# Kernel tuning notes

Hardware: AMD Instinct MI355X
Metric: run time of the kernel (lower is better)

## Reference

```python
import jax, jax.numpy as jnp
import numpy as np

N, K = 50000, 16          # nodes, max degree (subgraph size = K+1)
C_IN, C_HID, C_OUT = 128, 128, 64
T1, T2 = 1.0, 0.5         # evolution_times per layer (used via .item() in torch, i.e. constants)


def setup_inputs() -> dict:
    key = jax.random.key(0)
    kx, kw1, kw2, kd = jax.random.split(key, 4)
    n = jnp.arange(N)
    # distinct, non-self neighbor ids: (n + m_n * j) mod N, m_n*j <= 97*16 < N
    m = 1 + (n % 97)
    j = jnp.arange(1, K + 1)
    neighbors = ((n[:, None] + m[:, None] * j[None, :]) % N).astype(jnp.int32)  # [N,K]
    deg = jax.random.randint(kd, (N,), 4, K + 1)                                # variable degree 4..16
    nbr_mask = jnp.arange(K)[None, :] < deg[:, None]                            # [N,K] bool
    x = jax.random.normal(kx, (N, C_IN), dtype=jnp.float32)
    # xavier-uniform linear weights (bias=False in lin; separate bias param zeros-init)
    lim1 = float(np.sqrt(6.0 / (C_IN + C_HID)))
    lim2 = float(np.sqrt(6.0 / (C_HID + C_OUT)))
    W1 = jax.random.uniform(kw1, (C_HID, C_IN), jnp.float32, -lim1, lim1)
    W2 = jax.random.uniform(kw2, (C_OUT, C_HID), jnp.float32, -lim2, lim2)
    b1 = jnp.zeros((C_HID,), jnp.float32)
    b2 = jnp.zeros((C_OUT,), jnp.float32)
    return {"x": x, "neighbors": neighbors, "nbr_mask": nbr_mask,
            "W1": W1, "b1": b1, "W2": W2, "b2": b2}


def _star_evolution_weights(nbr_mask, t):
    """Per-node unitary-dilation evolution weights Re(G[0,:]) / sqrt(max eig(G G^H)).

    A_i is the star adjacency of the node's incident subgraph (size K+1);
    padded leaves are disconnected so their row-0 weight is exactly 0.
    """
    S = K + 1
    m = nbr_mask.astype(jnp.float32)                       # [N,K]
    A = jnp.zeros((nbr_mask.shape[0], S, S), jnp.float32)
    A = A.at[:, 0, 1:].set(m).at[:, 1:, 0].set(m)          # star adjacency [N,S,S]
    G = jax.vmap(jax.scipy.linalg.expm)((-1j * t) * A.astype(jnp.complex64))  # [N,S,S] c64
    # normalization by sqrt(max eigenvalue of G G^H) (== 1 up to fp error: G unitary)
    GGd = jnp.einsum('nij,nkj->nik', G, jnp.conj(G))
    smax = jnp.sqrt(jnp.max(jnp.linalg.eigvalsh(GGd), axis=-1))              # [N]
    # features are real, only real part of evolved features is kept:
    return jnp.real(G[:, 0, :]) / smax[:, None].astype(jnp.float32)          # [N,S]


def _conv(h, W, b, neighbors, nbr_mask, t):
    ht = h @ W.T                                             # [N,C'] lin (no bias)
    g0 = _star_evolution_weights(nbr_mask, t)                # [N,K+1]
    sub = jnp.concatenate([ht[:, None, :], ht[neighbors]], axis=1)  # [N,K+1,C']
    return jnp.einsum('ns,nsc->nc', g0, sub) + b


def reference(x, neighbors, nbr_mask, W1, b1, W2, b2):
    h = jax.nn.relu(_conv(x, W1, b1, neighbors, nbr_mask, T1))   # dropout: eval mode (no-op)
    o = _conv(h, W2, b2, neighbors, nbr_mask, T2)
    return jax.nn.log_softmax(o, axis=1)
```

## Files before the change

### kernel.cpp

```cpp
#include <hip/hip_runtime.h>
#include <hip/hip_bf16.h>


#define NN    50000
#define CIN   128
#define CHID  128
#define COUT  64
#define KNBR  16
#define TM    64
#define BLOCK 256

typedef unsigned short u16;
typedef unsigned int   u32;
typedef __attribute__((ext_vector_type(8))) short bf16x8;
typedef __attribute__((ext_vector_type(4))) float f32x4;

__device__ __forceinline__ u16 f2bf(float f) {
    __hip_bfloat16 h = __float2bfloat16(f);
    return *reinterpret_cast<u16*>(&h);
}
__device__ __forceinline__ uint4 pack8u(const float* __restrict__ p) {
    float tmp[8];
    *(float4*)(tmp)     = *(const float4*)(p);
    *(float4*)(tmp + 4) = *(const float4*)(p + 4);
    union { u16 h[8]; uint4 v; } r;
    #pragma unroll
    for (int i = 0; i < 8; ++i) r.h[i] = f2bf(tmp[i]);
    return r.v;
}

__device__ __forceinline__ int sw(int row, int g) { return (g ^ (row & 15)) << 3; }

#define WS_CC_OFF 65536

__global__ void wprep(const float* __restrict__ w1g,
                      const float* __restrict__ w2g,
                      uint4* __restrict__ wimg)
{
    int gid = blockIdx.x * BLOCK + threadIdx.x;
    if (gid < 2048) {
        int c = gid >> 4, kg = gid & 15;
        wimg[kg * 128 + c] = pack8u(w1g + c * CIN + kg * 8);
    } else if (gid < 3072) {
        int g2 = gid - 2048;
        int c = g2 >> 4, kg = g2 & 15;
        wimg[2048 + kg * 64 + c] = pack8u(w2g + c * CHID + kg * 8);
    }
}

__global__ void cprep(const int* __restrict__ maskg, float* __restrict__ cc)
{
    int n = blockIdx.x * BLOCK + threadIdx.x;
    if (n < NN) {
        int deg = 0;
        #pragma unroll
        for (int j = 0; j < KNBR; ++j) deg += (maskg[(size_t)n * KNBR + j] != 0);
        float sd = sqrtf((float)deg);
        cc[n]      = cosf(sd);
        cc[NN + n] = cosf(0.5f * sd);
    }
}

__global__ __launch_bounds__(BLOCK, 3)
void gcn_mfma(const float* __restrict__ xg,
              const uint4* __restrict__ wimg,
              const float* __restrict__ cc,
              const float* __restrict__ b1g,
              const float* __restrict__ b2g,
              float* __restrict__ out)
{
    __shared__ __align__(16) char region[17408 + 16384];
    u16*   xt  = (u16*)region;
    float* osc = (float*)region;
    u16*   ht  = (u16*)(region + 17408);

    __shared__ float c1v[TM], c2v[TM], b1l[CHID], b2l[COUT];
    __shared__ float pm[TM * 4], ps[TM * 4], lsev[TM];

    const int t  = threadIdx.x;
    const int w  = t >> 6;
    const int L  = t & 63;
    const int q  = L >> 4;
    const int lm = L & 15;
    const int m0 = blockIdx.x * TM;

    #pragma unroll
    for (int i = 0; i < 4; ++i) {
        int c = t + i * BLOCK;
        int row = c >> 4, g = c & 15;
        int gn = m0 + row;
        uint4 v = make_uint4(0u, 0u, 0u, 0u);
        if (gn < NN) v = pack8u(xg + (size_t)gn * CIN + (g << 3));
        *(uint4*)&xt[row * CIN + sw(row, g)] = v;
    }

    bf16x8 w1f[2][4];
    #pragma unroll
    for (int nt = 0; nt < 2; ++nt) {
        int c = w * 32 + nt * 16 + lm;
        #pragma unroll
        for (int k4 = 0; k4 < 4; ++k4)
            w1f[nt][k4] = *(const bf16x8*)&wimg[(k4 * 4 + q) * 128 + c];
    }

    if (t < CHID) b1l[t] = b1g[t];
    if (t < COUT) b2l[t] = b2g[t];
    if (t < TM) {
        int gn = m0 + t;
        c1v[t] = (gn < NN) ? cc[gn]      : 0.f;
        c2v[t] = (gn < NN) ? cc[NN + gn] : 0.f;
    }
    __syncthreads();

    f32x4 acc[4][2];
    #pragma unroll
    for (int i = 0; i < 4; ++i)
        #pragma unroll
        for (int nt = 0; nt < 2; ++nt)
            acc[i][nt] = (f32x4){0.f, 0.f, 0.f, 0.f};

    #pragma unroll
    for (int k4 = 0; k4 < 4; ++k4) {
        bf16x8 af[4];
        #pragma unroll
        for (int i = 0; i < 4; ++i) {
            int r = i * 16 + lm;
            af[i] = *(const bf16x8*)&xt[r * CIN + sw(r, k4 * 4 + q)];
        }
        #pragma unroll
        for (int i = 0; i < 4; ++i)
            #pragma unroll
            for (int nt = 0; nt < 2; ++nt)
                acc[i][nt] = __builtin_amdgcn_mfma_f32_16x16x32_bf16(
                    af[i], w1f[nt][k4], acc[i][nt], 0, 0, 0);
    }

    #pragma unroll
    for (int i = 0; i < 4; ++i) {
        #pragma unroll
        for (int nt = 0; nt < 2; ++nt) {
            int chan = w * 32 + nt * 16 + lm;
            float bb = b1l[chan];
            #pragma unroll
            for (int r = 0; r < 4; ++r) {
                int node = i * 16 + q * 4 + r;
                float h = fmaxf(fmaf(c1v[node], acc[i][nt][r], bb), 0.f);
                ht[node * CHID + sw(node, chan >> 3) + (chan & 7)] = f2bf(h);
            }
        }
    }

    bf16x8 w2f[4];
    {
        int c = w * 16 + lm;
        #pragma unroll
        for (int k4 = 0; k4 < 4; ++k4)
            w2f[k4] = *(const bf16x8*)&wimg[2048 + (k4 * 4 + q) * 64 + c];
    }
    __syncthreads();

    f32x4 a2[4];
    #pragma unroll
    for (int i = 0; i < 4; ++i) a2[i] = (f32x4){0.f, 0.f, 0.f, 0.f};

    #pragma unroll
    for (int k4 = 0; k4 < 4; ++k4) {
        bf16x8 af[4];
        #pragma unroll
        for (int i = 0; i < 4; ++i) {
            int r = i * 16 + lm;
            af[i] = *(const bf16x8*)&ht[r * CHID + sw(r, k4 * 4 + q)];
        }
        #pragma unroll
        for (int i = 0; i < 4; ++i)
            a2[i] = __builtin_amdgcn_mfma_f32_16x16x32_bf16(
                af[i], w2f[k4], a2[i], 0, 0, 0);
    }

    {
        int chan = w * 16 + lm;
        float bb = b2l[chan];
        #pragma unroll
        for (int i = 0; i < 4; ++i)
            #pragma unroll
            for (int r = 0; r < 4; ++r) {
                int node = i * 16 + q * 4 + r;
                osc[node * 68 + chan] = fmaf(c2v[node], a2[i][r], bb);
            }
    }
    __syncthreads();

    {
        int node = t >> 2, part = t & 3;
        float m = -1e30f;
        #pragma unroll
        for (int qq = 0; qq < 16; ++qq)
            m = fmaxf(m, osc[node * 68 + part * 16 + qq]);
        pm[node * 4 + part] = m;
    }
    __syncthreads();
    {
        int node = t >> 2, part = t & 3;
        float M = fmaxf(fmaxf(pm[node * 4], pm[node * 4 + 1]),
                        fmaxf(pm[node * 4 + 2], pm[node * 4 + 3]));
        float s = 0.f;
        #pragma unroll
        for (int qq = 0; qq < 16; ++qq)
            s += expf(osc[node * 68 + part * 16 + qq] - M);
        ps[node * 4 + part] = s;
        if (part == 0) pm[node * 4] = M;
    }
    __syncthreads();
    {
        int node = t >> 2, part = t & 3;
        if (part == 0)
            lsev[node] = pm[node * 4] +
                logf(ps[node * 4] + ps[node * 4 + 1] + ps[node * 4 + 2] + ps[node * 4 + 3]);
    }
    __syncthreads();

    for (int e4 = t; e4 < TM * COUT / 4; e4 += BLOCK) {
        int n = e4 >> 4;
        if (m0 + n >= NN) break;
        int c0 = (e4 & 15) << 2;
        float l = lsev[n];
        float4 v;
        v.x = osc[n * 68 + c0]     - l;
        v.y = osc[n * 68 + c0 + 1] - l;
        v.z = osc[n * 68 + c0 + 2] - l;
        v.w = osc[n * 68 + c0 + 3] - l;
        *(float4*)(out + (size_t)(m0 + n) * COUT + c0) = v;
    }
}

extern "C" void kernel_launch(void* const* d_in, const int* in_sizes, int n_in,
                              void* d_out, int out_size, void* d_ws, size_t ws_size,
                              hipStream_t stream) {
    const float* x   = (const float*)d_in[0];
    const int* mask  = (const int*)d_in[2];
    const float* w1  = (const float*)d_in[3];
    const float* b1  = (const float*)d_in[4];
    const float* w2  = (const float*)d_in[5];
    const float* b2  = (const float*)d_in[6];
    float* out = (float*)d_out;

    uint4* wimg = (uint4*)d_ws;
    float* cc   = (float*)((char*)d_ws + WS_CC_OFF);

    hipLaunchKernelGGL(wprep, dim3(12), dim3(BLOCK), 0, stream, w1, w2, wimg);
    hipLaunchKernelGGL(cprep, dim3((NN + BLOCK - 1) / BLOCK), dim3(BLOCK), 0, stream,
                       mask, cc);

    int grid = (NN + TM - 1) / TM;
    hipLaunchKernelGGL(gcn_mfma, dim3(grid), dim3(BLOCK), 0, stream,
                       x, wimg, cc, b1, b2, out);
}
```

Before: 97.16 us.

## Transpose MFMA operands, do log-softmax in registers, merge prep kernels

Merges the weight-packing and degree-cosine prep kernels into one launch. Swaps MFMA operand order so each lane's accumulators hold one node's channels, letting layer-2 outputs and the log-softmax reduction stay in registers with cross-lane shuffles. This drops the shared-memory output staging and several block barriers. It uses fast __expf/__logf intrinsics and reads biases straight from global memory, which may slightly change precision.

```diff
diff --git a/kernel.cpp b/kernel.cpp
--- a/kernel.cpp
+++ b/kernel.cpp
@@ -32,32 +32,35 @@
 __device__ __forceinline__ int sw(int row, int g) { return (g ^ (row & 15)) << 3; }
 
 #define WS_CC_OFF 65536
-
-__global__ void wprep(const float* __restrict__ w1g,
-                      const float* __restrict__ w2g,
-                      uint4* __restrict__ wimg)
+#define CC_BLOCKS 196
+
+__global__ void prep(const float* __restrict__ w1g,
+                     const float* __restrict__ w2g,
+                     const int* __restrict__ maskg,
+                     uint4* __restrict__ wimg,
+                     float* __restrict__ cc)
 {
-    int gid = blockIdx.x * BLOCK + threadIdx.x;
-    if (gid < 2048) {
-        int c = gid >> 4, kg = gid & 15;
-        wimg[kg * 128 + c] = pack8u(w1g + c * CIN + kg * 8);
-    } else if (gid < 3072) {
-        int g2 = gid - 2048;
-        int c = g2 >> 4, kg = g2 & 15;
-        wimg[2048 + kg * 64 + c] = pack8u(w2g + c * CHID + kg * 8);
-    }
-}
-
-__global__ void cprep(const int* __restrict__ maskg, float* __restrict__ cc)
-{
-    int n = blockIdx.x * BLOCK + threadIdx.x;
-    if (n < NN) {
-        int deg = 0;
-        #pragma unroll
-        for (int j = 0; j < KNBR; ++j) deg += (maskg[(size_t)n * KNBR + j] != 0);
-        float sd = sqrtf((float)deg);
-        cc[n]      = cosf(sd);
-        cc[NN + n] = cosf(0.5f * sd);
+    int b = blockIdx.x;
+    if (b < CC_BLOCKS) {
+        int n = b * BLOCK + threadIdx.x;
+        if (n < NN) {
+            int deg = 0;
+            #pragma unroll
+            for (int j = 0; j < KNBR; ++j) deg += (maskg[(size_t)n * KNBR + j] != 0);
+            float sd = sqrtf((float)deg);
+            cc[n]      = cosf(sd);
+            cc[NN + n] = cosf(0.5f * sd);
+        }
+    } else {
+        int gid = (b - CC_BLOCKS) * BLOCK + threadIdx.x;
+        if (gid < 2048) {
+            int c = gid >> 4, kg = gid & 15;
+            wimg[kg * 128 + c] = pack8u(w1g + c * CIN + kg * 8);
+        } else if (gid < 3072) {
+            int g2 = gid - 2048;
+            int c = g2 >> 4, kg = g2 & 15;
+            wimg[2048 + kg * 64 + c] = pack8u(w2g + c * CHID + kg * 8);
+        }
     }
 }
 
@@ -69,13 +72,8 @@
               const float* __restrict__ b2g,
               float* __restrict__ out)
 {
-    __shared__ __align__(16) char region[17408 + 16384];
-    u16*   xt  = (u16*)region;
-    float* osc = (float*)region;
-    u16*   ht  = (u16*)(region + 17408);
-
-    __shared__ float c1v[TM], c2v[TM], b1l[CHID], b2l[COUT];
-    __shared__ float pm[TM * 4], ps[TM * 4], lsev[TM];
+    __shared__ __align__(16) u16 xt[TM * CIN];
+    __shared__ __align__(16) u16 ht[TM * CHID];
 
     const int t  = threadIdx.x;
     const int w  = t >> 6;
@@ -96,140 +94,116 @@
 
     bf16x8 w1f[2][4];
     #pragma unroll
-    for (int nt = 0; nt < 2; ++nt) {
-        int c = w * 32 + nt * 16 + lm;
+    for (int mt = 0; mt < 2; ++mt) {
+        int c = (2 * w + mt) * 16 + lm;
         #pragma unroll
         for (int k4 = 0; k4 < 4; ++k4)
-            w1f[nt][k4] = *(const bf16x8*)&wimg[(k4 * 4 + q) * 128 + c];
-    }
-
-    if (t < CHID) b1l[t] = b1g[t];
-    if (t < COUT) b2l[t] = b2g[t];
-    if (t < TM) {
-        int gn = m0 + t;
-        c1v[t] = (gn < NN) ? cc[gn]      : 0.f;
-        c2v[t] = (gn < NN) ? cc[NN + gn] : 0.f;
+            w1f[mt][k4] = *(const bf16x8*)&wimg[(k4 * 4 + q) * 128 + c];
+    }
+    float c1n[4];
+    #pragma unroll
+    for (int nt = 0; nt < 4; ++nt) {
+        int gn = m0 + nt * 16 + lm;
+        c1n[nt] = (gn < NN) ? cc[gn] : 0.f;
     }
     __syncthreads();
 
-    f32x4 acc[4][2];
-    #pragma unroll
-    for (int i = 0; i < 4; ++i)
-        #pragma unroll
-        for (int nt = 0; nt < 2; ++nt)
-            acc[i][nt] = (f32x4){0.f, 0.f, 0.f, 0.f};
+    f32x4 acc[2][4];
+    #pragma unroll
+    for (int mt = 0; mt < 2; ++mt)
+        #pragma unroll
+        for (int nt = 0; nt < 4; ++nt)
+            acc[mt][nt] = (f32x4){0.f, 0.f, 0.f, 0.f};
 
     #pragma unroll
     for (int k4 = 0; k4 < 4; ++k4) {
-        bf16x8 af[4];
-        #pragma unroll
-        for (int i = 0; i < 4; ++i) {
-            int r = i * 16 + lm;
-            af[i] = *(const bf16x8*)&xt[r * CIN + sw(r, k4 * 4 + q)];
-        }
-        #pragma unroll
-        for (int i = 0; i < 4; ++i)
+        bf16x8 xf[4];
+        #pragma unroll
+        for (int nt = 0; nt < 4; ++nt) {
+            int r = nt * 16 + lm;
+            xf[nt] = *(const bf16x8*)&xt[r * CIN + sw(r, k4 * 4 + q)];
+        }
+        #pragma unroll
+        for (int mt = 0; mt < 2; ++mt)
             #pragma unroll
-            for (int nt = 0; nt < 2; ++nt)
-                acc[i][nt] = __builtin_amdgcn_mfma_f32_16x16x32_bf16(
-                    af[i], w1f[nt][k4], acc[i][nt], 0, 0, 0);
-    }
-
-    #pragma unroll
-    for (int i = 0; i < 4; ++i) {
-        #pragma unroll
-        for (int nt = 0; nt < 2; ++nt) {
-            int chan = w * 32 + nt * 16 + lm;
-            float bb = b1l[chan];
-            #pragma unroll
-            for (int r = 0; r < 4; ++r) {
-                int node = i * 16 + q * 4 + r;
-                float h = fmaxf(fmaf(c1v[node], acc[i][nt][r], bb), 0.f);
-                ht[node * CHID + sw(node, chan >> 3) + (chan & 7)] = f2bf(h);
-            }
-        }
-    }
-
-    bf16x8 w2f[4];
-    {
-        int c = w * 16 + lm;
+            for (int nt = 0; nt < 4; ++nt)
+                acc[mt][nt] = __builtin_amdgcn_mfma_f32_16x16x32_bf16(
+                    w1f[mt][k4], xf[nt], acc[mt][nt], 0, 0, 0);
+    }
+
+    #pragma unroll
+    for (int mt = 0; mt < 2; ++mt) {
+        int chan0 = (2 * w + mt) * 16 + q * 4;
+        float4 bb = *(const float4*)(b1g + chan0);
+        #pragma unroll
+        for (int nt = 0; nt < 4; ++nt) {
+            int node = nt * 16 + lm;
+            float c1 = c1n[nt];
+            u16 h0 = f2bf(fmaxf(fmaf(c1, acc[mt][nt][0], bb.x), 0.f));
+            u16 h1 = f2bf(fmaxf(fmaf(c1, acc[mt][nt][1], bb.y), 0.f));
+            u16 h2 = f2bf(fmaxf(fmaf(c1, acc[mt][nt][2], bb.z), 0.f));
+            u16 h3 = f2bf(fmaxf(fmaf(c1, acc[mt][nt][3], bb.w), 0.f));
+            uint2 pkt = make_uint2(((u32)h0) | ((u32)h1 << 16),
+                                   ((u32)h2) | ((u32)h3 << 16));
+            *(uint2*)&ht[node * CHID + sw(node, chan0 >> 3) + (chan0 & 7)] = pkt;
+        }
+    }
+    __syncthreads();
+
+    const int node = 16 * w + lm;
+    const int gn   = m0 + node;
+
+    bf16x8 hf[4];
+    #pragma unroll
+    for (int k4 = 0; k4 < 4; ++k4)
+        hf[k4] = *(const bf16x8*)&ht[node * CHID + sw(node, k4 * 4 + q)];
+
+    float o[4][4];
+    float c2 = (gn < NN) ? cc[NN + gn] : 0.f;
+    #pragma unroll
+    for (int mt = 0; mt < 4; ++mt) {
+        bf16x8 w2f[4];
         #pragma unroll
         for (int k4 = 0; k4 < 4; ++k4)
-            w2f[k4] = *(const bf16x8*)&wimg[2048 + (k4 * 4 + q) * 64 + c];
-    }
-    __syncthreads();
-
-    f32x4 a2[4];
-    #pragma unroll
-    for (int i = 0; i < 4; ++i) a2[i] = (f32x4){0.f, 0.f, 0.f, 0.f};
-
-    #pragma unroll
-    for (int k4 = 0; k4 < 4; ++k4) {
-        bf16x8 af[4];
-        #pragma unroll
-        for (int i = 0; i < 4; ++i) {
-            int r = i * 16 + lm;
-            af[i] = *(const bf16x8*)&ht[r * CHID + sw(r, k4 * 4 + q)];
-        }
-        #pragma unroll
-        for (int i = 0; i < 4; ++i)
-            a2[i] = __builtin_amdgcn_mfma_f32_16x16x32_bf16(
-                af[i], w2f[k4], a2[i], 0, 0, 0);
-    }
-
-    {
-        int chan = w * 16 + lm;
-        float bb = b2l[chan];
-        #pragma unroll
-        for (int i = 0; i < 4; ++i)
-            #pragma unroll
-            for (int r = 0; r < 4; ++r) {
-                int node = i * 16 + q * 4 + r;
-                osc[node * 68 + chan] = fmaf(c2v[node], a2[i][r], bb);
-            }
-    }
-    __syncthreads();
-
-    {
-        int node = t >> 2, part = t & 3;
-        float m = -1e30f;
-        #pragma unroll
-        for (int qq = 0; qq < 16; ++qq)
-            m = fmaxf(m, osc[node * 68 + part * 16 + qq]);
-        pm[node * 4 + part] = m;
-    }
-    __syncthreads();
-    {
-        int node = t >> 2, part = t & 3;
-        float M = fmaxf(fmaxf(pm[node * 4], pm[node * 4 + 1]),
-                        fmaxf(pm[node * 4 + 2], pm[node * 4 + 3]));
-        float s = 0.f;
-        #pragma unroll
-        for (int qq = 0; qq < 16; ++qq)
-            s += expf(osc[node * 68 + part * 16 + qq] - M);
-        ps[node * 4 + part] = s;
-        if (part == 0) pm[node * 4] = M;
-    }
-    __syncthreads();
-    {
-        int node = t >> 2, part = t & 3;
-        if (part == 0)
-            lsev[node] = pm[node * 4] +
-                logf(ps[node * 4] + ps[node * 4 + 1] + ps[node * 4 + 2] + ps[node * 4 + 3]);
-    }
-    __syncthreads();
-
-    for (int e4 = t; e4 < TM * COUT / 4; e4 += BLOCK) {
-        int n = e4 >> 4;
-        if (m0 + n >= NN) break;
-        int c0 = (e4 & 15) << 2;
-        float l = lsev[n];
-        float4 v;
-        v.x = osc[n * 68 + c0]     - l;
-        v.y = osc[n * 68 + c0 + 1] - l;
-        v.z = osc[n * 68 + c0 + 2] - l;
-        v.w = osc[n * 68 + c0 + 3] - l;
-        *(float4*)(out + (size_t)(m0 + n) * COUT + c0) = v;
+            w2f[k4] = *(const bf16x8*)&wimg[2048 + (k4 * 4 + q) * 64 + (mt * 16 + lm)];
+        f32x4 a2 = (f32x4){0.f, 0.f, 0.f, 0.f};
+        #pragma unroll
+        for (int k4 = 0; k4 < 4; ++k4)
+            a2 = __builtin_amdgcn_mfma_f32_16x16x32_bf16(w2f[k4], hf[k4], a2, 0, 0, 0);
+        float4 bb = *(const float4*)(b2g + mt * 16 + q * 4);
+        o[mt][0] = fmaf(c2, a2[0], bb.x);
+        o[mt][1] = fmaf(c2, a2[1], bb.y);
+        o[mt][2] = fmaf(c2, a2[2], bb.z);
+        o[mt][3] = fmaf(c2, a2[3], bb.w);
+    }
+
+    float M = -1e30f;
+    #pragma unroll
+    for (int mt = 0; mt < 4; ++mt)
+        #pragma unroll
+        for (int r = 0; r < 4; ++r) M = fmaxf(M, o[mt][r]);
+    M = fmaxf(M, __shfl_xor(M, 16));
+    M = fmaxf(M, __shfl_xor(M, 32));
+
+    float S = 0.f;
+    #pragma unroll
+    for (int mt = 0; mt < 4; ++mt)
+        #pragma unroll
+        for (int r = 0; r < 4; ++r) S += __expf(o[mt][r] - M);
+    S += __shfl_xor(S, 16);
+    S += __shfl_xor(S, 32);
+    float lse = M + __logf(S);
+
+    if (gn < NN) {
+        #pragma unroll
+        for (int mt = 0; mt < 4; ++mt) {
+            float4 v;
+            v.x = o[mt][0] - lse;
+            v.y = o[mt][1] - lse;
+            v.z = o[mt][2] - lse;
+            v.w = o[mt][3] - lse;
+            *(float4*)(out + (size_t)gn * COUT + mt * 16 + q * 4) = v;
+        }
     }
 }
 
@@ -247,9 +221,8 @@
     uint4* wimg = (uint4*)d_ws;
     float* cc   = (float*)((char*)d_ws + WS_CC_OFF);
 
-    hipLaunchKernelGGL(wprep, dim3(12), dim3(BLOCK), 0, stream, w1, w2, wimg);
-    hipLaunchKernelGGL(cprep, dim3((NN + BLOCK - 1) / BLOCK), dim3(BLOCK), 0, stream,
-                       mask, cc);
+    hipLaunchKernelGGL(prep, dim3(CC_BLOCKS + 12), dim3(BLOCK), 0, stream,
+                       w1, w2, mask, wimg, cc);
 
     int grid = (NN + TM - 1) / TM;
     hipLaunchKernelGGL(gcn_mfma, dim3(grid), dim3(BLOCK), 0, stream,
```

Result: faster. 92.09 us (-5.2%).
